# Kernel tuning notes

Measured on AMD Instinct MI355X. Metric: run time of the kernel, lower is better.

Reference implementation:

```python
import jax, jax.numpy as jnp
import numpy as np

B, N, M, D, V = 16, 2048, 2048, 128, 128


def setup_inputs() -> dict:
    key0 = jax.random.key(0)
    kq, kk, kv, kp = jax.random.split(key0, 4)
    return {
        "query": jax.random.normal(kq, (B, N, D), dtype=jnp.float32),
        "key": jax.random.normal(kk, (B, M, D), dtype=jnp.float32),
        "value": jax.random.normal(kv, (B, M, V), dtype=jnp.float32),
        "key_padding_len": jax.random.randint(kp, (B,), 0, 512),
        "is_attn_mask_len": 1,  # Python int -> causal masking on
    }


def reference(query, key, value, key_padding_len, is_attn_mask_len):
    # query:[B,N,D], key:[B,M,D], value:[B,M,V], key_padding_len:[B]
    Bq, Nq, Dq = query.shape
    Mk = key.shape[1]
    scale = 1.0 / jnp.sqrt(jnp.asarray(Dq, dtype=query.dtype))

    # torch mask(): zero out the LAST key_padding_len key positions
    pos = jnp.arange(Mk)
    keep = pos[None, :] < (Mk - key_padding_len)[:, None]  # [B,M]
    key = jnp.where(keep[:, :, None], key, jnp.zeros((), key.dtype))

    score = jnp.einsum("bnd,bmd->bnm", query, key) * scale  # [B,N,M]

    if is_attn_mask_len:
        # attn_mask_len[b,i] = M-1-i  ->  row i keeps positions j <= i (causal)
        causal = pos[None, :] <= jnp.arange(Nq)[:, None]  # [N,M]
        score = jnp.where(causal[None, :, :], score, jnp.asarray(-1e6, score.dtype))

    attn = jax.nn.softmax(score, axis=-1)  # dropout p=0 -> identity
    out = jnp.einsum("bnm,bmv->bnv", attn, value)  # [B,N,V]
    return out
```

## Files before the change

kernel.cpp:

```cpp
#include <hip/hip_runtime.h>
#include <stdint.h>

typedef unsigned short ushort_t;
typedef __attribute__((ext_vector_type(8))) short short8;
typedef __attribute__((ext_vector_type(4))) float floatx4;

#define SEQ_N 2048
#define SEQ_M 2048
#define DIM_D 128
#define DIM_V 128
#define BC 64

#define KS_LD 136
#define VS_LD 72
#define PS_LD 72
#define KB(i) ((i) * 8704)
#define VB(i) (17408 + (i) * 9216)
#define P0 35840
#define SMEM_ELEMS 40448

#define WS_O_FLOATS (256 * 2 * 64 * 128)
#define WS_M_OFF    WS_O_FLOATS
#define WS_L_OFF    (WS_O_FLOATS + 32768)
#define WS_FLOATS   (WS_O_FLOATS + 65536)

#if __has_builtin(__builtin_amdgcn_exp2f)
#define EXP2F(x) __builtin_amdgcn_exp2f(x)
#else
#define EXP2F(x) exp2f(x)
#endif

template <int CTRL>
__device__ __forceinline__ float dpp_f(float x) {
  int xi = __builtin_bit_cast(int, x);
  int yi = __builtin_amdgcn_update_dpp(xi, xi, CTRL, 0xf, 0xf, false);
  return __builtin_bit_cast(float, yi);
}
__device__ __forceinline__ float rowmax16(float x) {
  x = fmaxf(x, dpp_f<0x128>(x));
  x = fmaxf(x, dpp_f<0x124>(x));
  x = fmaxf(x, dpp_f<0x122>(x));
  x = fmaxf(x, dpp_f<0x121>(x));
  return x;
}
__device__ __forceinline__ float rowsum16(float x) {
  x += dpp_f<0x128>(x);
  x += dpp_f<0x124>(x);
  x += dpp_f<0x122>(x);
  x += dpp_f<0x121>(x);
  return x;
}

__device__ __forceinline__ ushort_t f2bf(float f) {
  uint32_t u = __builtin_bit_cast(uint32_t, f);
  return (ushort_t)((u + 0x8000u) >> 16);
}
__device__ __forceinline__ uint32_t bfpack(float lo, float hi) {
  uint32_t a = __builtin_bit_cast(uint32_t, lo) + 0x8000u;
  uint32_t b = __builtin_bit_cast(uint32_t, hi) + 0x8000u;
  return __builtin_amdgcn_perm(b, a, 0x07060302u);
}

__device__ __forceinline__ void process_chunk(
    const float* __restrict__ Q, const float* __restrict__ K,
    const float* __restrict__ Vg, float* __restrict__ Out,
    float* __restrict__ ws, ushort_t* __restrict__ smem,
    int b, int rt, int jt_lo, int jt_hi, int mlimit, int flag, int c, bool direct) {
  const int tid  = threadIdx.x;
  const int lane = tid & 63;
  const int w    = tid >> 6;
  const int qd   = lane >> 4;
  const int nn   = lane & 15;

  const float c1 = 0.08838834764831845f * 1.4426950408889634f;

  const int oct = tid & 15;
  const int j0  = (tid >> 4) * 4;
  const int hh  = nn >> 3;
  const int rb  = 8 * hh;

  const int i0w = rt * 64 + w * 16;
  const size_t koff = (size_t)b * SEQ_M * DIM_D;
  const size_t voff = (size_t)b * SEQ_M * DIM_V;

  short8 qf[4];
  {
    const float* Qb = Q + ((size_t)b * SEQ_N + (size_t)(i0w + nn)) * DIM_D;
    union { short8 v; uint32_t u32[4]; } t;
#pragma unroll
    for (int ks = 0; ks < 4; ++ks) {
      const float* p = Qb + ks * 32 + qd * 8;
      float4 f0 = *(const float4*)p, f1 = *(const float4*)(p + 4);
      t.u32[0] = bfpack(f0.x, f0.y);
      t.u32[1] = bfpack(f0.z, f0.w);
      t.u32[2] = bfpack(f1.x, f1.y);
      t.u32[3] = bfpack(f1.z, f1.w);
      qf[ks] = t.v;
    }
  }

  floatx4 o[8];
#pragma unroll
  for (int vt = 0; vt < 8; ++vt) o[vt] = (floatx4)0.0f;
  float m[4], l[4];
#pragma unroll
  for (int r = 0; r < 4; ++r) { m[r] = -3.0e38f; l[r] = 0.0f; }

  float4 kr[4][2], vr[4][2];

  auto stage_load = [&](int jt) {
    const int jbase = jt * BC;
#pragma unroll
    for (int r = 0; r < 4; ++r) {
      const float* kp = K  + koff + (size_t)(jbase + j0 + r) * DIM_D + oct * 8;
      kr[r][0] = *(const float4*)kp;  kr[r][1] = *(const float4*)(kp + 4);
      const float* vp = Vg + voff + (size_t)(jbase + j0 + r) * DIM_V + oct * 8;
      vr[r][0] = *(const float4*)vp;  vr[r][1] = *(const float4*)(vp + 4);
    }
  };

  auto stage_write = [&](int buf, int jt) {
    const int jbase = jt * BC;
    const int kb = KB(buf), vb = VB(buf);
#pragma unroll
    for (int r = 0; r < 4; ++r) {
      uint4 kw;
      kw.x = bfpack(kr[r][0].x, kr[r][0].y);
      kw.y = bfpack(kr[r][0].z, kr[r][0].w);
      kw.z = bfpack(kr[r][1].x, kr[r][1].y);
      kw.w = bfpack(kr[r][1].z, kr[r][1].w);
      if (jbase + j0 + r >= mlimit) kw = make_uint4(0u, 0u, 0u, 0u);
      *(uint4*)(smem + kb + (j0 + r) * KS_LD + oct * 8) = kw;
    }
    float vc[4][8];
#pragma unroll
    for (int r = 0; r < 4; ++r) {
      vc[r][0]=vr[r][0].x; vc[r][1]=vr[r][0].y; vc[r][2]=vr[r][0].z; vc[r][3]=vr[r][0].w;
      vc[r][4]=vr[r][1].x; vc[r][5]=vr[r][1].y; vc[r][6]=vr[r][1].z; vc[r][7]=vr[r][1].w;
    }
#pragma unroll
    for (int q = 0; q < 8; ++q) {
      const int p = 8 * oct + ((oct + q) & 7);
      uint2 dv;
      dv.x = bfpack(vc[0][q], vc[1][q]);
      dv.y = bfpack(vc[2][q], vc[3][q]);
      *(uint2*)(smem + vb + p * VS_LD + j0) = dv;
    }
  };

  stage_load(jt_lo);
  stage_write(0, jt_lo);
  __syncthreads();

  const int len = jt_hi - jt_lo;
#pragma unroll 1
  for (int t = 0; t < len; ++t) {
    const int jt = jt_lo + t;
    const int cur = t & 1;
    const bool more = (t + 1) < len;
    const int jbase = jt * BC;
    if (more) stage_load(jt + 1);

    const int kb = KB(cur), vb = VB(cur);

    floatx4 s[4];
#pragma unroll
    for (int ct = 0; ct < 4; ++ct) s[ct] = (floatx4)0.0f;
#pragma unroll
    for (int ks = 0; ks < 4; ++ks) {
#pragma unroll
      for (int ct = 0; ct < 4; ++ct) {
        short8 bf = *(const short8*)(smem + kb + (ct * 16 + nn) * KS_LD + ks * 32 + qd * 8);
        s[ct] = __builtin_amdgcn_mfma_f32_16x16x32_bf16(qf[ks], bf, s[ct], 0, 0, 0);
      }
    }

    {
      float tt[4][4];
      const bool needmask = flag && (jbase + BC - 1 > i0w);
#pragma unroll
      for (int ct = 0; ct < 4; ++ct)
#pragma unroll
        for (int r = 0; r < 4; ++r) {
          float tv = s[ct][r] * c1;
          if (needmask) {
            int jgl = jbase + ct * 16 + nn;
            int igl = i0w + qd * 4 + r;
            if (jgl > igl) tv = -3.0e38f;
          }
          tt[ct][r] = tv;
        }
#pragma unroll
      for (int r = 0; r < 4; ++r) {
        float mr = fmaxf(fmaxf(tt[0][r], tt[1][r]), fmaxf(tt[2][r], tt[3][r]));
        mr = rowmax16(mr);
        float mn = fmaxf(m[r], mr);
        float alpha = EXP2F(m[r] - mn);
        m[r] = mn;
        float ps = 0.0f;
#pragma unroll
        for (int ct = 0; ct < 4; ++ct) {
          float p = EXP2F(tt[ct][r] - mn);
          tt[ct][r] = p;
          ps += p;
        }
        l[r] = l[r] * alpha + ps;
#pragma unroll
        for (int vt = 0; vt < 8; ++vt) o[vt][r] *= alpha;
      }
#pragma unroll
      for (int ct = 0; ct < 4; ++ct)
#pragma unroll
        for (int r = 0; r < 4; ++r)
          smem[P0 + (w * 16 + qd * 4 + r) * PS_LD + ct * 16 + nn] = f2bf(tt[ct][r]);
    }

#pragma unroll
    for (int ks2 = 0; ks2 < 2; ++ks2) {
      short8 a = *(const short8*)(smem + P0 + (w * 16 + nn) * PS_LD + ks2 * 32 + qd * 8);
#pragma unroll
      for (int vt = 0; vt < 8; ++vt) {
        const int p = 16 * vt + rb + ((2 * vt + nn + hh) & 7);
        short8 vbf = *(const short8*)(smem + vb + p * VS_LD + ks2 * 32 + qd * 8);
        o[vt] = __builtin_amdgcn_mfma_f32_16x16x32_bf16(a, vbf, o[vt], 0, 0, 0);
      }
    }

    if (more) stage_write(cur ^ 1, jt + 1);
    __syncthreads();
  }

#pragma unroll
  for (int r = 0; r < 4; ++r) l[r] = rowsum16(l[r]);

  if (direct) {
    float* Ob = Out + ((size_t)b * SEQ_N + i0w) * DIM_V;
#pragma unroll
    for (int r = 0; r < 4; ++r) {
      float inv = 1.0f / l[r];
      int row = qd * 4 + r;
#pragma unroll
      for (int vt = 0; vt < 8; ++vt)
        Ob[(size_t)row * DIM_V + vt * 16 + nn] = o[vt][r] * inv;
    }
  } else {
    const int p = b * 16 + (rt - 16);
    const int slot = p * 2 + c;
    float* Op = ws + (size_t)slot * 64 * 128;
#pragma unroll
    for (int r = 0; r < 4; ++r) {
      int row = w * 16 + qd * 4 + r;
#pragma unroll
      for (int vt = 0; vt < 8; ++vt)
        Op[(size_t)row * 128 + vt * 16 + nn] = o[vt][r];
    }
    if (nn == 0) {
#pragma unroll
      for (int r = 0; r < 4; ++r) {
        int row = w * 16 + qd * 4 + r;
        ws[WS_M_OFF + slot * 64 + row] = m[r];
        ws[WS_L_OFF + slot * 64 + row] = l[r];
      }
    }
  }
}

__global__ __launch_bounds__(256, 2)
void fa_chunk(const float* __restrict__ Q, const float* __restrict__ K,
              const float* __restrict__ Vg, const int* __restrict__ kpl,
              const int* __restrict__ amask, float* __restrict__ Out,
              float* __restrict__ ws) {
  __shared__ __align__(16) ushort_t smem[SMEM_ELEMS];
  const int bx = blockIdx.x;
  const int b  = bx & 15;
  const int u  = bx >> 4;
  int rt, c;
  if (u < 16)      { rt = 16 + u; c = 0; }
  else if (u < 32) { rt = 47 - u; c = 1; }
  else             { rt = 47 - u; c = 0; }
  const int flag   = amask[0];
  const int mlimit = SEQ_M - kpl[b];
  const int ntiles = flag ? (rt + 1) : (SEQ_M / BC);
  const int jt_lo  = (c == 1) ? 16 : 0;
  const int jt_hi  = (c == 0 && rt >= 16) ? 16 : ntiles;
  process_chunk(Q, K, Vg, Out, ws, smem, b, rt, jt_lo, jt_hi, mlimit, flag, c, rt < 16);
}

__global__ __launch_bounds__(256)
void fa_merge(const float* __restrict__ ws, float* __restrict__ Out) {
  const int w = threadIdx.x >> 6, lane = threadIdx.x & 63;
  const int rowid = blockIdx.x * 4 + w;
  const int p = rowid >> 6, rr = rowid & 63;
  const int b = p >> 4, rt = 16 + (p & 15);
  float m1 = ws[WS_M_OFF + (p * 2 + 0) * 64 + rr];
  float l1 = ws[WS_L_OFF + (p * 2 + 0) * 64 + rr];
  float m2 = ws[WS_M_OFF + (p * 2 + 1) * 64 + rr];
  float l2 = ws[WS_L_OFF + (p * 2 + 1) * 64 + rr];
  float M  = fmaxf(m1, m2);
  float a1 = EXP2F(m1 - M), a2 = EXP2F(m2 - M);
  float inv = 1.0f / (l1 * a1 + l2 * a2);
  const float* O1 = ws + ((size_t)(p * 2 + 0) * 64 + rr) * 128;
  const float* O2 = ws + ((size_t)(p * 2 + 1) * 64 + rr) * 128;
  float2 x1 = *(const float2*)(O1 + lane * 2);
  float2 x2 = *(const float2*)(O2 + lane * 2);
  float2 r;
  r.x = (x1.x * a1 + x2.x * a2) * inv;
  r.y = (x1.y * a1 + x2.y * a2) * inv;
  *(float2*)(Out + ((size_t)b * SEQ_N + rt * 64 + rr) * 128 + lane * 2) = r;
}

__global__ __launch_bounds__(256, 2)
void fa_paired(const float* __restrict__ Q, const float* __restrict__ K,
               const float* __restrict__ Vg, const int* __restrict__ kpl,
               const int* __restrict__ amask, float* __restrict__ Out) {
  __shared__ __align__(16) ushort_t smem[SMEM_ELEMS];
  const int bx = blockIdx.x;
  const int b  = bx & 15;
  const int pp = bx >> 4;
  const int flag   = amask[0];
  const int mlimit = SEQ_M - kpl[b];
#pragma unroll 1
  for (int ph = 0; ph < 2; ++ph) {
    const int rt = ph ? (31 - pp) : pp;
    const int ntiles = flag ? (rt + 1) : (SEQ_M / BC);
    process_chunk(Q, K, Vg, Out, nullptr, smem, b, rt, 0, ntiles, mlimit, flag, 0, true);
  }
}

extern "C" void kernel_launch(void* const* d_in, const int* in_sizes, int n_in,
                              void* d_out, int out_size, void* d_ws, size_t ws_size,
                              hipStream_t stream) {
  const float* Q   = (const float*)d_in[0];
  const float* K   = (const float*)d_in[1];
  const float* V   = (const float*)d_in[2];
  const int* kpl   = (const int*)d_in[3];
  const int* amask = (const int*)d_in[4];
  float* O         = (float*)d_out;
  float* ws        = (float*)d_ws;

  if (ws_size >= (size_t)WS_FLOATS * 4) {
    hipLaunchKernelGGL(fa_chunk, dim3(768), dim3(256), 0, stream, Q, K, V, kpl, amask, O, ws);
    hipLaunchKernelGGL(fa_merge, dim3(4096), dim3(256), 0, stream, ws, O);
  } else {
    hipLaunchKernelGGL(fa_paired, dim3(256), dim3(256), 0, stream, Q, K, V, kpl, amask, O);
  }
}
```

Baseline: 149.2 us.

## Add bf16 K/V-transposed prep pass and 128-row split-KV flash attention kernel

```diff
diff --git a/kernel.cpp b/kernel.cpp
--- a/kernel.cpp
+++ b/kernel.cpp
@@ -10,6 +10,336 @@
 #define DIM_D 128
 #define DIM_V 128
 #define BC 64
+
+
+#if __has_builtin(__builtin_amdgcn_exp2f)
+#define EXP2F(x) __builtin_amdgcn_exp2f(x)
+#else
+#define EXP2F(x) exp2f(x)
+#endif
+
+template <int CTRL>
+__device__ __forceinline__ float dpp_f(float x) {
+  int xi = __builtin_bit_cast(int, x);
+  int yi = __builtin_amdgcn_update_dpp(xi, xi, CTRL, 0xf, 0xf, false);
+  return __builtin_bit_cast(float, yi);
+}
+__device__ __forceinline__ float rowmax16(float x) {
+  x = fmaxf(x, dpp_f<0x128>(x));
+  x = fmaxf(x, dpp_f<0x124>(x));
+  x = fmaxf(x, dpp_f<0x122>(x));
+  x = fmaxf(x, dpp_f<0x121>(x));
+  return x;
+}
+__device__ __forceinline__ float rowsum16(float x) {
+  x += dpp_f<0x128>(x);
+  x += dpp_f<0x124>(x);
+  x += dpp_f<0x122>(x);
+  x += dpp_f<0x121>(x);
+  return x;
+}
+
+__device__ __forceinline__ ushort_t f2bf(float f) {
+  uint32_t u = __builtin_bit_cast(uint32_t, f);
+  return (ushort_t)((u + 0x8000u) >> 16);
+}
+__device__ __forceinline__ uint32_t bfpack(float lo, float hi) {
+  uint32_t a = __builtin_bit_cast(uint32_t, lo) + 0x8000u;
+  uint32_t b = __builtin_bit_cast(uint32_t, hi) + 0x8000u;
+  return __builtin_amdgcn_perm(b, a, 0x07060302u);
+}
+
+#define BM2 128
+#define K2OFF 0
+#define V2OFF 16384
+#define P2OFF 32768
+#define SMEM2 40960
+#define KELEMS 8192
+#define VELEMS 8192
+
+#define WS2_KB 0
+#define WS2_VT 2097152
+#define WS2_PO 4194304
+#define WS2_M  8388608
+#define WS2_L  8454144
+#define WS2_FLOATS 8519680
+
+__device__ __forceinline__ void stage16(const ushort_t* src, ushort_t* lds_base, int lane) {
+#if __has_builtin(__builtin_amdgcn_global_load_lds)
+  __builtin_amdgcn_global_load_lds(
+      (const __attribute__((address_space(1))) void*)src,
+      (__attribute__((address_space(3))) void*)lds_base, 16, 0, 0);
+#else
+  *(uint4*)(lds_base + lane * 8) = *(const uint4*)src;
+#endif
+}
+
+__global__ __launch_bounds__(256)
+void prep2(const float* __restrict__ K, const float* __restrict__ Vg,
+           const int* __restrict__ kpl, float* __restrict__ ws) {
+  __shared__ __align__(16) ushort_t lt[64][72];
+  ushort_t* Kb = (ushort_t*)(ws + WS2_KB);
+  ushort_t* Vt = (ushort_t*)(ws + WS2_VT);
+  const int g = blockIdx.x, tid = threadIdx.x;
+  if (g < 2048) {
+    const size_t e = (size_t)g * 2048 + (size_t)tid * 8;
+    const int row = (int)(e >> 7);
+    const int b = row >> 11, mm = row & 2047;
+    const int mlimit = SEQ_M - kpl[b];
+    uint4 kw = make_uint4(0u, 0u, 0u, 0u);
+    if (mm < mlimit) {
+      const float* p = K + e;
+      float4 f0 = *(const float4*)p, f1 = *(const float4*)(p + 4);
+      kw.x = bfpack(f0.x, f0.y); kw.y = bfpack(f0.z, f0.w);
+      kw.z = bfpack(f1.x, f1.y); kw.w = bfpack(f1.z, f1.w);
+    }
+    *(uint4*)(Kb + e) = kw;
+  } else {
+    const int g2 = g - 2048;
+    const int b = g2 >> 6;
+    const int mt = (g2 & 63) >> 1;
+    const int vh = (g2 & 1) * 64;
+    const int mrow = tid >> 2, v0 = (tid & 3) * 16;
+    const float* p = Vg + ((size_t)b * SEQ_M + (size_t)(mt * 64 + mrow)) * DIM_V + vh + v0;
+    float4 f0 = *(const float4*)p, f1 = *(const float4*)(p + 4);
+    float4 f2 = *(const float4*)(p + 8), f3 = *(const float4*)(p + 12);
+    lt[v0 +  0][mrow] = f2bf(f0.x); lt[v0 +  1][mrow] = f2bf(f0.y);
+    lt[v0 +  2][mrow] = f2bf(f0.z); lt[v0 +  3][mrow] = f2bf(f0.w);
+    lt[v0 +  4][mrow] = f2bf(f1.x); lt[v0 +  5][mrow] = f2bf(f1.y);
+    lt[v0 +  6][mrow] = f2bf(f1.z); lt[v0 +  7][mrow] = f2bf(f1.w);
+    lt[v0 +  8][mrow] = f2bf(f2.x); lt[v0 +  9][mrow] = f2bf(f2.y);
+    lt[v0 + 10][mrow] = f2bf(f2.z); lt[v0 + 11][mrow] = f2bf(f2.w);
+    lt[v0 + 12][mrow] = f2bf(f3.x); lt[v0 + 13][mrow] = f2bf(f3.y);
+    lt[v0 + 14][mrow] = f2bf(f3.z); lt[v0 + 15][mrow] = f2bf(f3.w);
+    __syncthreads();
+    const int v = tid >> 2, mo = (tid & 3) * 16;
+    ushort_t* dst = Vt + ((size_t)(b * DIM_V + vh + v) * SEQ_M) + mt * 64 + mo;
+    *(uint4*)(dst + 0) = *(const uint4*)&lt[v][mo];
+    *(uint4*)(dst + 8) = *(const uint4*)&lt[v][mo + 8];
+  }
+}
+
+__global__ __launch_bounds__(512, 4)
+void fa2(const float* __restrict__ Q, const int* __restrict__ amask,
+         float* __restrict__ Out, float* __restrict__ ws) {
+  __shared__ __align__(16) ushort_t sm[SMEM2];
+  const ushort_t* __restrict__ Kb = (const ushort_t*)(ws + WS2_KB);
+  const ushort_t* __restrict__ Vt = (const ushort_t*)(ws + WS2_VT);
+
+  const int tid = threadIdx.x;
+  const int lane = tid & 63;
+  const int w = tid >> 6;
+  const int qd = lane >> 4;
+  const int nn = lane & 15;
+
+  const int bx = blockIdx.x;
+  const int xcd = bx & 7;
+  const int q8 = bx >> 3;
+  const int b = xcd * 2 + (q8 & 1);
+  const int u = q8 >> 1;
+  const int c = (u >= 16) ? 1 : 0;
+  const int rt = c ? (31 - u) : (15 - u);
+
+  const int flag = amask[0];
+  const int ntf = flag ? (2 * rt + 2) : (SEQ_M / BC);
+  const int sp  = flag ? (rt + 1) : (SEQ_M / BC / 2);
+  const int jt_lo = c ? sp : 0;
+  const int jt_hi = c ? ntf : sp;
+
+  const int i0w = rt * BM2 + w * 16;
+  const float c1 = 0.08838834764831845f * 1.4426950408889634f;
+
+  short8 qf[4];
+  {
+    const float* Qb = Q + ((size_t)b * SEQ_N + (size_t)(i0w + nn)) * DIM_D;
+    union { short8 v; uint32_t u32[4]; } tq;
+#pragma unroll
+    for (int ks = 0; ks < 4; ++ks) {
+      const float* p = Qb + ks * 32 + qd * 8;
+      float4 f0 = *(const float4*)p, f1 = *(const float4*)(p + 4);
+      tq.u32[0] = bfpack(f0.x, f0.y);
+      tq.u32[1] = bfpack(f0.z, f0.w);
+      tq.u32[2] = bfpack(f1.x, f1.y);
+      tq.u32[3] = bfpack(f1.z, f1.w);
+      qf[ks] = tq.v;
+    }
+  }
+
+  floatx4 o[8];
+#pragma unroll
+  for (int vt = 0; vt < 8; ++vt) o[vt] = (floatx4)0.0f;
+  float m[4], l[4];
+#pragma unroll
+  for (int r = 0; r < 4; ++r) { m[r] = -3.0e38f; l[r] = 0.0f; }
+
+  const size_t kbatch = (size_t)b * (SEQ_M * DIM_D);
+  const size_t vbatch = (size_t)b * ((size_t)DIM_V * SEQ_M);
+
+  auto stage = [&](int buf, int jt) {
+    const int jb = jt * BC;
+#pragma unroll
+    for (int i = 0; i < 2; ++i) {
+      const int seg = w + 8 * i;
+      {
+        const int rrow = seg * 4 + (lane >> 4);
+        const int col  = (lane & 15) * 8;
+        const ushort_t* src = Kb + kbatch + ((size_t)(jb + rrow) << 7)
+                              + (col ^ ((rrow & 7) << 3));
+        stage16(src, &sm[K2OFF + buf * KELEMS + seg * 512], lane);
+      }
+      {
+        const int vrow = seg * 8 + (lane >> 3);
+        const int col  = (lane & 7) * 8;
+        const ushort_t* src = Vt + vbatch + ((size_t)vrow << 11) + jb
+                              + (col ^ ((vrow & 7) << 3));
+        stage16(src, &sm[V2OFF + buf * VELEMS + seg * 512], lane);
+      }
+    }
+  };
+
+  stage(0, jt_lo);
+  __syncthreads();
+
+  const int len = jt_hi - jt_lo;
+  const int swl = (nn & 7) << 3;
+#pragma unroll 1
+  for (int t = 0; t < len; ++t) {
+    const int cur = t & 1;
+    const int jbase = (jt_lo + t) * BC;
+    if (t + 1 < len) stage(cur ^ 1, jt_lo + t + 1);
+
+    const int kb = K2OFF + cur * KELEMS;
+    const int vb = V2OFF + cur * VELEMS;
+
+    floatx4 s[4];
+#pragma unroll
+    for (int ct = 0; ct < 4; ++ct) s[ct] = (floatx4)0.0f;
+    __builtin_amdgcn_s_setprio(1);
+#pragma unroll
+    for (int ks = 0; ks < 4; ++ks) {
+#pragma unroll
+      for (int ct = 0; ct < 4; ++ct) {
+        short8 bf = *(const short8*)&sm[kb + (ct * 16 + nn) * 128
+                                        + ((ks * 32 + qd * 8) ^ swl)];
+        s[ct] = __builtin_amdgcn_mfma_f32_16x16x32_bf16(qf[ks], bf, s[ct], 0, 0, 0);
+      }
+    }
+    __builtin_amdgcn_s_setprio(0);
+
+    {
+      const bool needmask = flag && (jbase + BC - 1 > i0w);
+      if (needmask) {
+#pragma unroll
+        for (int ct = 0; ct < 4; ++ct) {
+          const int jgl = jbase + ct * 16 + nn;
+#pragma unroll
+          for (int r = 0; r < 4; ++r) {
+            float tv = s[ct][r] * c1;
+            s[ct][r] = (jgl > i0w + qd * 4 + r) ? -3.0e38f : tv;
+          }
+        }
+      } else {
+#pragma unroll
+        for (int ct = 0; ct < 4; ++ct)
+#pragma unroll
+          for (int r = 0; r < 4; ++r) s[ct][r] *= c1;
+      }
+#pragma unroll
+      for (int r = 0; r < 4; ++r) {
+        float mr = fmaxf(fmaxf(s[0][r], s[1][r]), fmaxf(s[2][r], s[3][r]));
+        mr = rowmax16(mr);
+        const float mn = fmaxf(m[r], mr);
+        const float alpha = EXP2F(m[r] - mn);
+        m[r] = mn;
+        const int prow = w * 16 + qd * 4 + r;
+        const int psw = ((qd * 4 + r) & 7) << 3;
+        float ps = 0.0f;
+#pragma unroll
+        for (int ct = 0; ct < 4; ++ct) {
+          float p = EXP2F(s[ct][r] - mn);
+          ps += p;
+          sm[P2OFF + prow * 64 + ((ct * 16 + nn) ^ psw)] = f2bf(p);
+        }
+        l[r] = l[r] * alpha + ps;
+#pragma unroll
+        for (int vt = 0; vt < 8; ++vt) o[vt][r] *= alpha;
+      }
+    }
+
+    __builtin_amdgcn_s_setprio(1);
+#pragma unroll
+    for (int ks2 = 0; ks2 < 2; ++ks2) {
+      short8 a = *(const short8*)&sm[P2OFF + (w * 16 + nn) * 64
+                                     + ((ks2 * 32 + qd * 8) ^ swl)];
+#pragma unroll
+      for (int vt = 0; vt < 8; ++vt) {
+        short8 vbf = *(const short8*)&sm[vb + (vt * 16 + nn) * 64
+                                         + ((ks2 * 32 + qd * 8) ^ swl)];
+        o[vt] = __builtin_amdgcn_mfma_f32_16x16x32_bf16(a, vbf, o[vt], 0, 0, 0);
+      }
+    }
+    __builtin_amdgcn_s_setprio(0);
+
+    __syncthreads();
+  }
+
+#pragma unroll
+  for (int r = 0; r < 4; ++r) l[r] = rowsum16(l[r]);
+
+  const int rb = b * 16 + rt;
+  if (c == 0) {
+    float* Od = Out + ((size_t)b * SEQ_N + i0w) * DIM_V;
+#pragma unroll
+    for (int r = 0; r < 4; ++r) {
+      const int row = qd * 4 + r;
+#pragma unroll
+      for (int vt = 0; vt < 8; ++vt)
+        Od[(size_t)row * DIM_V + vt * 16 + nn] = o[vt][r];
+    }
+  } else {
+    float* Od = ws + WS2_PO + (size_t)rb * (BM2 * DIM_V);
+#pragma unroll
+    for (int r = 0; r < 4; ++r) {
+      const int row = w * 16 + qd * 4 + r;
+#pragma unroll
+      for (int vt = 0; vt < 8; ++vt)
+        Od[(size_t)row * DIM_V + vt * 16 + nn] = o[vt][r];
+    }
+  }
+  if (nn == 0) {
+    const int slot = rb * 2 + c;
+#pragma unroll
+    for (int r = 0; r < 4; ++r) {
+      const int row = w * 16 + qd * 4 + r;
+      ws[WS2_M + slot * 128 + row] = m[r];
+      ws[WS2_L + slot * 128 + row] = l[r];
+    }
+  }
+}
+
+__global__ __launch_bounds__(256)
+void fa2_merge(float* __restrict__ Out, const float* __restrict__ ws) {
+  const int w = threadIdx.x >> 6, lane = threadIdx.x & 63;
+  const int rowid = blockIdx.x * 4 + w;
+  const int rb = rowid >> 7, rr = rowid & 127;
+  const int b = rb >> 4, rt = rb & 15;
+  const float m1 = ws[WS2_M + (rb * 2 + 0) * 128 + rr];
+  const float l1 = ws[WS2_L + (rb * 2 + 0) * 128 + rr];
+  const float m2 = ws[WS2_M + (rb * 2 + 1) * 128 + rr];
+  const float l2 = ws[WS2_L + (rb * 2 + 1) * 128 + rr];
+  const float M = fmaxf(m1, m2);
+  const float a1 = EXP2F(m1 - M), a2 = EXP2F(m2 - M);
+  const float inv = 1.0f / (l1 * a1 + l2 * a2);
+  float* O1 = Out + ((size_t)b * SEQ_N + (size_t)rt * BM2 + rr) * DIM_V;
+  const float* O2 = ws + WS2_PO + ((size_t)rb * (BM2 * DIM_V) + (size_t)rr * DIM_V);
+  float2 x1 = *(const float2*)(O1 + lane * 2);
+  float2 x2 = *(const float2*)(O2 + lane * 2);
+  float2 r;
+  r.x = (x1.x * a1 + x2.x * a2) * inv;
+  r.y = (x1.y * a1 + x2.y * a2) * inv;
+  *(float2*)(O1 + lane * 2) = r;
+}
+
 
 #define KS_LD 136
 #define VS_LD 72
@@ -23,43 +353,6 @@
 #define WS_M_OFF    WS_O_FLOATS
 #define WS_L_OFF    (WS_O_FLOATS + 32768)
 #define WS_FLOATS   (WS_O_FLOATS + 65536)
-
-#if __has_builtin(__builtin_amdgcn_exp2f)
-#define EXP2F(x) __builtin_amdgcn_exp2f(x)
-#else
-#define EXP2F(x) exp2f(x)
-#endif
-
-template <int CTRL>
-__device__ __forceinline__ float dpp_f(float x) {
-  int xi = __builtin_bit_cast(int, x);
-  int yi = __builtin_amdgcn_update_dpp(xi, xi, CTRL, 0xf, 0xf, false);
-  return __builtin_bit_cast(float, yi);
-}
-__device__ __forceinline__ float rowmax16(float x) {
-  x = fmaxf(x, dpp_f<0x128>(x));
-  x = fmaxf(x, dpp_f<0x124>(x));
-  x = fmaxf(x, dpp_f<0x122>(x));
-  x = fmaxf(x, dpp_f<0x121>(x));
-  return x;
-}
-__device__ __forceinline__ float rowsum16(float x) {
-  x += dpp_f<0x128>(x);
-  x += dpp_f<0x124>(x);
-  x += dpp_f<0x122>(x);
-  x += dpp_f<0x121>(x);
-  return x;
-}
-
-__device__ __forceinline__ ushort_t f2bf(float f) {
-  uint32_t u = __builtin_bit_cast(uint32_t, f);
-  return (ushort_t)((u + 0x8000u) >> 16);
-}
-__device__ __forceinline__ uint32_t bfpack(float lo, float hi) {
-  uint32_t a = __builtin_bit_cast(uint32_t, lo) + 0x8000u;
-  uint32_t b = __builtin_bit_cast(uint32_t, hi) + 0x8000u;
-  return __builtin_amdgcn_perm(b, a, 0x07060302u);
-}
 
 __device__ __forceinline__ void process_chunk(
     const float* __restrict__ Q, const float* __restrict__ K,
@@ -338,7 +631,11 @@
   float* O         = (float*)d_out;
   float* ws        = (float*)d_ws;
 
-  if (ws_size >= (size_t)WS_FLOATS * 4) {
+  if (ws_size >= (size_t)WS2_FLOATS * 4) {
+    hipLaunchKernelGGL(prep2, dim3(3072), dim3(256), 0, stream, K, V, kpl, ws);
+    hipLaunchKernelGGL(fa2, dim3(512), dim3(512), 0, stream, Q, amask, O, ws);
+    hipLaunchKernelGGL(fa2_merge, dim3(8192), dim3(256), 0, stream, O, ws);
+  } else if (ws_size >= (size_t)WS_FLOATS * 4) {
     hipLaunchKernelGGL(fa_chunk, dim3(768), dim3(256), 0, stream, Q, K, V, kpl, amask, O, ws);
     hipLaunchKernelGGL(fa_merge, dim3(4096), dim3(256), 0, stream, ws, O);
   } else {
```

New measurement: 171.5 us. 1.15x slower.
